# Performance work log

Hardware: AMD Instinct MI355X
Metric: run time of the kernel (lower is better)

The kernel has to match this reference:

```python
import jax, jax.numpy as jnp
import numpy as np

BATCH = 65536
INPUT_DIM = 128
NUM_PROTOTYPES = 512
OUTPUT_DIM = 8


def setup_inputs() -> dict:
    key = jax.random.key(0)
    k1, k2, k3 = jax.random.split(key, 3)
    x = jax.random.normal(k1, (BATCH, INPUT_DIM), dtype=jnp.float32)
    prototypes = jax.random.normal(k2, (NUM_PROTOTYPES, INPUT_DIM), dtype=jnp.float32)
    prototype_outputs = jax.random.normal(k3, (NUM_PROTOTYPES, OUTPUT_DIM), dtype=jnp.float32)
    relevance = jnp.ones((INPUT_DIM,), dtype=jnp.float32)
    return {"x": x, "prototypes": prototypes, "prototype_outputs": prototype_outputs, "relevance": relevance}


def reference(x, prototypes, prototype_outputs, relevance):
    # dist[b,p] = sum_d r2[d] * (x[b,d] - proto[p,d])^2
    # Expanded to avoid materializing the (B, P, D) broadcast tensor:
    #   = sum_d r2*x^2 + sum_d r2*p^2 - 2 * sum_d x * r2 * p
    r2 = relevance ** 2                                   # [D]
    x_sq = (x * x) @ r2                                   # [B]
    p_sq = (prototypes * prototypes) @ r2                 # [P]
    cross = x @ (prototypes * r2).T                       # [B, P]
    dist = x_sq[:, None] + p_sq[None, :] - 2.0 * cross    # [B, P]
    idx = jnp.argmin(dist, axis=1)                        # [B]
    return prototype_outputs[idx]                         # [B, output_dim]
```

## Files before the change

### kernel.cpp

```cpp
#include <hip/hip_runtime.h>

#define BATCH 65536
#define DIM 128
#define NPROTO 512
#define ODIM 8

#define ROWS 128
#define THREADS 512


__global__ void grlvq_prep_w(const float* __restrict__ proto,
                             const float* __restrict__ rel,
                             float* __restrict__ wT) {
    const int tid = blockIdx.x * 256 + threadIdx.x;
    const int p = tid >> 5, c = tid & 31;
    const int wb = p >> 6, oo = (p >> 3) & 7, j = p & 7;
    float4 rv = *(const float4*)(rel + c * 4);
    float4 pv = *(const float4*)(proto + (size_t)p * DIM + c * 4);
    float4 o;
    o.x = pv.x * (rv.x * rv.x);
    o.y = pv.y * (rv.y * rv.y);
    o.z = pv.z * (rv.z * rv.z);
    o.w = pv.w * (rv.w * rv.w);
    *(float4*)(wT + wb * 8192 + oo * 1024 + c * 32 + j * 4) = o;
}

__global__ void grlvq_prep_psq(const float* __restrict__ proto,
                               const float* __restrict__ rel,
                               float* __restrict__ psq) {
    const int p = blockIdx.x * 64 + threadIdx.x;
    float acc = 0.f;
    #pragma unroll 8
    for (int c = 0; c < 32; ++c) {
        float4 rv = *(const float4*)(rel + c * 4);
        float4 pv = *(const float4*)(proto + (size_t)p * DIM + c * 4);
        float r2;
        r2 = rv.x * rv.x; acc = fmaf(r2 * pv.x, pv.x, acc);
        r2 = rv.y * rv.y; acc = fmaf(r2 * pv.y, pv.y, acc);
        r2 = rv.z * rv.z; acc = fmaf(r2 * pv.z, pv.z, acc);
        r2 = rv.w * rv.w; acc = fmaf(r2 * pv.w, pv.w, acc);
    }
    psq[p] = acc;
}

__global__ __launch_bounds__(THREADS, 4) void grlvq_main(const float* __restrict__ x,
                                                         const float* __restrict__ wT,
                                                         const float* __restrict__ psq,
                                                         const float* __restrict__ pout,
                                                         float* __restrict__ out) {
    __shared__ __align__(16) char smem[65536];
    float4* xs4  = (float4*)smem;
    float*  red_s = (float*)smem;
    int*    red_i = (int*)(smem + 4096);

    const int t = threadIdx.x;
    const int rowBase = blockIdx.x * ROWS;

    {
        const int r = t & 127;
        const int cbase = t >> 7;
        const float4* xg = (const float4*)(x + (size_t)(rowBase + r) * DIM);
        #pragma unroll
        for (int k = 0; k < 8; ++k) {
            const int c = cbase + 4 * k;
            xs4[c * 128 + r] = xg[c];
        }
    }
    __syncthreads();

    const int lane = t & 63;
    const int wid  = __builtin_amdgcn_readfirstlane(t >> 6);
    const float* wbase = wT + (size_t)wid * 8192;
    const int pbase = wid * 64;

    float bestA = INFINITY, bestB = INFINITY;
    int idxA = pbase, idxB = pbase;

    #pragma unroll 1
    for (int oo2 = 0; oo2 < 4; ++oo2) {
        float accA[16], accB[16];
        #pragma unroll
        for (int j = 0; j < 16; ++j) { accA[j] = 0.f; accB[j] = 0.f; }

        const float* wp0 = wbase + oo2 * 2048;
        const float* wp1 = wp0 + 1024;
        #pragma unroll 8
        for (int c = 0; c < 32; ++c) {
            float4 xa = xs4[c * 128 + lane];
            float4 xb = xs4[c * 128 + lane + 64];
            const float* wc0 = wp0 + c * 32;
            const float* wc1 = wp1 + c * 32;
            #pragma unroll
            for (int j = 0; j < 8; ++j) {
                float w0 = wc0[j * 4 + 0], w1 = wc0[j * 4 + 1];
                float w2 = wc0[j * 4 + 2], w3 = wc0[j * 4 + 3];
                accA[j] = fmaf(xa.x, w0, accA[j]);
                accA[j] = fmaf(xa.y, w1, accA[j]);
                accA[j] = fmaf(xa.z, w2, accA[j]);
                accA[j] = fmaf(xa.w, w3, accA[j]);
                accB[j] = fmaf(xb.x, w0, accB[j]);
                accB[j] = fmaf(xb.y, w1, accB[j]);
                accB[j] = fmaf(xb.z, w2, accB[j]);
                accB[j] = fmaf(xb.w, w3, accB[j]);
            }
            #pragma unroll
            for (int j = 0; j < 8; ++j) {
                float w0 = wc1[j * 4 + 0], w1 = wc1[j * 4 + 1];
                float w2 = wc1[j * 4 + 2], w3 = wc1[j * 4 + 3];
                accA[8 + j] = fmaf(xa.x, w0, accA[8 + j]);
                accA[8 + j] = fmaf(xa.y, w1, accA[8 + j]);
                accA[8 + j] = fmaf(xa.z, w2, accA[8 + j]);
                accA[8 + j] = fmaf(xa.w, w3, accA[8 + j]);
                accB[8 + j] = fmaf(xb.x, w0, accB[8 + j]);
                accB[8 + j] = fmaf(xb.y, w1, accB[8 + j]);
                accB[8 + j] = fmaf(xb.z, w2, accB[8 + j]);
                accB[8 + j] = fmaf(xb.w, w3, accB[8 + j]);
            }
        }

        #pragma unroll
        for (int j = 0; j < 16; ++j) {
            float pq = psq[pbase + oo2 * 16 + j];
            float sA = pq - 2.0f * accA[j];
            float sB = pq - 2.0f * accB[j];
            if (sA < bestA) { bestA = sA; idxA = pbase + oo2 * 16 + j; }
            if (sB < bestB) { bestB = sB; idxB = pbase + oo2 * 16 + j; }
        }
    }

    __syncthreads();

    red_s[lane * 8 + wid] = bestA;        red_i[lane * 8 + wid] = idxA;
    red_s[(lane + 64) * 8 + wid] = bestB; red_i[(lane + 64) * 8 + wid] = idxB;
    __syncthreads();

    if (t < ROWS) {
        float b = INFINITY;
        int bi = 0;
        #pragma unroll
        for (int w8 = 0; w8 < 8; ++w8) {
            float s = red_s[t * 8 + w8];
            int  id = red_i[t * 8 + w8];
            if (s < b) { b = s; bi = id; }
        }
        const float4* po = (const float4*)(pout + (size_t)bi * ODIM);
        float4* op = (float4*)(out + (size_t)(rowBase + t) * ODIM);
        op[0] = po[0];
        op[1] = po[1];
    }
}

extern "C" void kernel_launch(void* const* d_in, const int* in_sizes, int n_in,
                              void* d_out, int out_size, void* d_ws, size_t ws_size,
                              hipStream_t stream) {
    const float* x     = (const float*)d_in[0];
    const float* proto = (const float*)d_in[1];
    const float* pout  = (const float*)d_in[2];
    const float* rel   = (const float*)d_in[3];
    float* out = (float*)d_out;

    float* wT  = (float*)d_ws;
    float* psq = wT + NPROTO * DIM;

    grlvq_prep_w<<<64, 256, 0, stream>>>(proto, rel, wT);
    grlvq_prep_psq<<<8, 64, 0, stream>>>(proto, rel, psq);
    grlvq_main<<<BATCH / ROWS, THREADS, 0, stream>>>(x, wT, psq, pout, out);
}
```

Measured before the change: 171.7 us.

## Stage relevance-weighted prototype chunks in shared memory for block-wide reuse

Changes the prototype weight layout to dimension-major and has each block cooperatively load 128-prototype chunks into LDS. All waves then read their 16 prototypes per chunk as float4 LDS broadcasts instead of per-wave scalar global loads. The goal is to cut global/cache traffic for the weight operand. The cost is much larger LDS use, one block per CU, and extra barriers per chunk. It also adds a lowest-index tie-break in the final argmin reduction.

```diff
diff --git a/kernel.cpp b/kernel.cpp
--- a/kernel.cpp
+++ b/kernel.cpp
@@ -7,14 +7,14 @@
 
 #define ROWS 128
 #define THREADS 512
+#define CHUNK 128
 
 
 __global__ void grlvq_prep_w(const float* __restrict__ proto,
                              const float* __restrict__ rel,
-                             float* __restrict__ wT) {
+                             float* __restrict__ wTg) {
     const int tid = blockIdx.x * 256 + threadIdx.x;
-    const int p = tid >> 5, c = tid & 31;
-    const int wb = p >> 6, oo = (p >> 3) & 7, j = p & 7;
+    const int c = tid >> 9, p = tid & 511;
     float4 rv = *(const float4*)(rel + c * 4);
     float4 pv = *(const float4*)(proto + (size_t)p * DIM + c * 4);
     float4 o;
@@ -22,7 +22,7 @@
     o.y = pv.y * (rv.y * rv.y);
     o.z = pv.z * (rv.z * rv.z);
     o.w = pv.w * (rv.w * rv.w);
-    *(float4*)(wT + wb * 8192 + oo * 1024 + c * 32 + j * 4) = o;
+    ((float4*)wTg)[c * 512 + p] = o;
 }
 
 __global__ void grlvq_prep_psq(const float* __restrict__ proto,
@@ -43,15 +43,15 @@
     psq[p] = acc;
 }
 
-__global__ __launch_bounds__(THREADS, 4) void grlvq_main(const float* __restrict__ x,
-                                                         const float* __restrict__ wT,
+__global__ __launch_bounds__(THREADS, 1) void grlvq_main(const float* __restrict__ x,
+                                                         const float* __restrict__ wTg,
                                                          const float* __restrict__ psq,
                                                          const float* __restrict__ pout,
                                                          float* __restrict__ out) {
-    __shared__ __align__(16) char smem[65536];
-    float4* xs4  = (float4*)smem;
-    float*  red_s = (float*)smem;
-    int*    red_i = (int*)(smem + 4096);
+    __shared__ __align__(16) float4 xs4[32 * 128];
+    __shared__ __align__(16) float4 ws4[32 * CHUNK];
+    __shared__ float red_s[ROWS * 8];
+    __shared__ int   red_i[ROWS * 8];
 
     const int t = threadIdx.x;
     const int rowBase = blockIdx.x * ROWS;
@@ -66,82 +66,72 @@
             xs4[c * 128 + r] = xg[c];
         }
     }
-    __syncthreads();
 
     const int lane = t & 63;
     const int wid  = __builtin_amdgcn_readfirstlane(t >> 6);
-    const float* wbase = wT + (size_t)wid * 8192;
-    const int pbase = wid * 64;
+    const float4* wTg4 = (const float4*)wTg;
 
     float bestA = INFINITY, bestB = INFINITY;
-    int idxA = pbase, idxB = pbase;
+    int idxA = 0, idxB = 0;
 
     #pragma unroll 1
-    for (int oo2 = 0; oo2 < 4; ++oo2) {
+    for (int ch = 0; ch < NPROTO / CHUNK; ++ch) {
+        __syncthreads();
+        #pragma unroll
+        for (int k = 0; k < 8; ++k) {
+            const int idx = t + k * THREADS;
+            const int c = idx >> 7, pl = idx & 127;
+            ws4[c * 128 + pl] = wTg4[c * 512 + ch * CHUNK + pl];
+        }
+        __syncthreads();
+
         float accA[16], accB[16];
         #pragma unroll
         for (int j = 0; j < 16; ++j) { accA[j] = 0.f; accB[j] = 0.f; }
 
-        const float* wp0 = wbase + oo2 * 2048;
-        const float* wp1 = wp0 + 1024;
-        #pragma unroll 8
+        #pragma unroll 4
         for (int c = 0; c < 32; ++c) {
             float4 xa = xs4[c * 128 + lane];
             float4 xb = xs4[c * 128 + lane + 64];
-            const float* wc0 = wp0 + c * 32;
-            const float* wc1 = wp1 + c * 32;
+            const float4* wrow = &ws4[c * 128 + wid * 16];
             #pragma unroll
-            for (int j = 0; j < 8; ++j) {
-                float w0 = wc0[j * 4 + 0], w1 = wc0[j * 4 + 1];
-                float w2 = wc0[j * 4 + 2], w3 = wc0[j * 4 + 3];
-                accA[j] = fmaf(xa.x, w0, accA[j]);
-                accA[j] = fmaf(xa.y, w1, accA[j]);
-                accA[j] = fmaf(xa.z, w2, accA[j]);
-                accA[j] = fmaf(xa.w, w3, accA[j]);
-                accB[j] = fmaf(xb.x, w0, accB[j]);
-                accB[j] = fmaf(xb.y, w1, accB[j]);
-                accB[j] = fmaf(xb.z, w2, accB[j]);
-                accB[j] = fmaf(xb.w, w3, accB[j]);
-            }
-            #pragma unroll
-            for (int j = 0; j < 8; ++j) {
-                float w0 = wc1[j * 4 + 0], w1 = wc1[j * 4 + 1];
-                float w2 = wc1[j * 4 + 2], w3 = wc1[j * 4 + 3];
-                accA[8 + j] = fmaf(xa.x, w0, accA[8 + j]);
-                accA[8 + j] = fmaf(xa.y, w1, accA[8 + j]);
-                accA[8 + j] = fmaf(xa.z, w2, accA[8 + j]);
-                accA[8 + j] = fmaf(xa.w, w3, accA[8 + j]);
-                accB[8 + j] = fmaf(xb.x, w0, accB[8 + j]);
-                accB[8 + j] = fmaf(xb.y, w1, accB[8 + j]);
-                accB[8 + j] = fmaf(xb.z, w2, accB[8 + j]);
-                accB[8 + j] = fmaf(xb.w, w3, accB[8 + j]);
+            for (int j = 0; j < 16; ++j) {
+                float4 wv = wrow[j];
+                accA[j] = fmaf(xa.x, wv.x, accA[j]);
+                accA[j] = fmaf(xa.y, wv.y, accA[j]);
+                accA[j] = fmaf(xa.z, wv.z, accA[j]);
+                accA[j] = fmaf(xa.w, wv.w, accA[j]);
+                accB[j] = fmaf(xb.x, wv.x, accB[j]);
+                accB[j] = fmaf(xb.y, wv.y, accB[j]);
+                accB[j] = fmaf(xb.z, wv.z, accB[j]);
+                accB[j] = fmaf(xb.w, wv.w, accB[j]);
             }
         }
 
         #pragma unroll
         for (int j = 0; j < 16; ++j) {
-            float pq = psq[pbase + oo2 * 16 + j];
+            const int p = ch * CHUNK + wid * 16 + j;
+            float pq = psq[p];
             float sA = pq - 2.0f * accA[j];
             float sB = pq - 2.0f * accB[j];
-            if (sA < bestA) { bestA = sA; idxA = pbase + oo2 * 16 + j; }
-            if (sB < bestB) { bestB = sB; idxB = pbase + oo2 * 16 + j; }
+            if (sA < bestA) { bestA = sA; idxA = p; }
+            if (sB < bestB) { bestB = sB; idxB = p; }
         }
     }
 
     __syncthreads();
-
     red_s[lane * 8 + wid] = bestA;        red_i[lane * 8 + wid] = idxA;
     red_s[(lane + 64) * 8 + wid] = bestB; red_i[(lane + 64) * 8 + wid] = idxB;
     __syncthreads();
 
     if (t < ROWS) {
         float b = INFINITY;
-        int bi = 0;
+        int bi = 0x7fffffff;
         #pragma unroll
         for (int w8 = 0; w8 < 8; ++w8) {
             float s = red_s[t * 8 + w8];
             int  id = red_i[t * 8 + w8];
-            if (s < b) { b = s; bi = id; }
+            if (s < b || (s == b && id < bi)) { b = s; bi = id; }
         }
         const float4* po = (const float4*)(pout + (size_t)bi * ODIM);
         float4* op = (float4*)(out + (size_t)(rowBase + t) * ODIM);
@@ -159,10 +149,10 @@
     const float* rel   = (const float*)d_in[3];
     float* out = (float*)d_out;
 
-    float* wT  = (float*)d_ws;
-    float* psq = wT + NPROTO * DIM;
+    float* wTg = (float*)d_ws;
+    float* psq = wTg + NPROTO * DIM;
 
-    grlvq_prep_w<<<64, 256, 0, stream>>>(proto, rel, wT);
+    grlvq_prep_w<<<64, 256, 0, stream>>>(proto, rel, wTg);
     grlvq_prep_psq<<<8, 64, 0, stream>>>(proto, rel, psq);
-    grlvq_main<<<BATCH / ROWS, THREADS, 0, stream>>>(x, wT, psq, pout, out);
+    grlvq_main<<<BATCH / ROWS, THREADS, 0, stream>>>(x, wTg, psq, pout, out);
 }
```

New measurement: 214.2 us. +24.7%, slower.
